# Kernel optimization log

Hardware: AMD Instinct MI355X
Metric: run time of the kernel (lower is better)

## Reference

```python
import jax, jax.numpy as jnp
import numpy as np

B, L, D, H, DH, MAX_SEQ = 2, 2048, 512, 8, 64, 2048


def setup_inputs() -> dict:
    key = jax.random.key(0)
    ks = jax.random.split(key, 9)
    w = 0.02
    return {
        "q": jax.random.normal(ks[0], (B, L, D), jnp.float32),
        "k": jax.random.normal(ks[1], (B, L, D), jnp.float32),
        "v": jax.random.normal(ks[2], (B, L, D), jnp.float32),
        "Wq_w": jax.random.normal(ks[3], (D, D), jnp.float32) * w,
        "Wq_b": jnp.zeros((D,), jnp.float32),
        "Wk_w": jax.random.normal(ks[4], (D, D), jnp.float32) * w,
        "Wk_b": jnp.zeros((D,), jnp.float32),
        "Wv_w": jax.random.normal(ks[5], (D, D), jnp.float32) * w,
        "Wv_b": jnp.zeros((D,), jnp.float32),
        "fc_w": jax.random.normal(ks[6], (D, D), jnp.float32) * w,
        "fc_b": jnp.zeros((D,), jnp.float32),
        "E": jax.random.normal(ks[7], (MAX_SEQ, DH), jnp.float32),
        "mask": jnp.triu(jnp.ones((L, L), jnp.int32), k=1)[None, None],  # 1 = masked
    }


def reference(q, k, v, Wq_w, Wq_b, Wk_w, Wk_b, Wv_w, Wv_b, fc_w, fc_b, E, mask):
    b, lq, d = q.shape

    def proj(x, w, bias):
        # torch Linear: x @ W.T + b, then split heads -> [b, h, l, dh]
        y = x @ w.T + bias
        return y.reshape(b, -1, H, DH).transpose(0, 2, 1, 3)

    qh, kh, vh = proj(q, Wq_w, Wq_b), proj(k, Wk_w, Wk_b), proj(v, Wv_w, Wv_b)
    len_q, len_k = qh.shape[2], kh.shape[2]

    # relative embedding slice (starting_point = max(0, max_seq - len_q))
    e = E[max(0, MAX_SEQ - len_q):, :]          # [m, dh], m == len_q here
    m = e.shape[0]

    QE = jnp.einsum('bhld,md->bhlm', qh, e)      # [b,h,lq,m]
    # qe_masking: keep column j of row i iff j >= m-1-i
    keep = (jnp.arange(m)[None, :] >= (m - 1 - jnp.arange(len_q))[:, None])
    QE = QE * keep.astype(QE.dtype)

    # skewing: left-pad last dim, reshape swapping trailing dims, drop first row
    padded = jnp.pad(QE, ((0, 0), (0, 0), (0, 0), (1, 0)))      # [b,h,lq,m+1]
    Srel = padded.reshape(b, H, m + 1, len_q)[:, :, 1:, :]       # [b,h,m,lq]
    if len_k > len_q:
        Srel = jnp.pad(Srel, ((0, 0), (0, 0), (0, len_k - len_q), (0, 0)))
    elif len_k < len_q:
        Srel = Srel[:, :, :, :len_k]

    QKt = jnp.einsum('bhld,bhmd->bhlm', qh, kh)                  # [b,h,lq,lk]
    logits = (QKt + Srel) / jnp.sqrt(jnp.float32(DH))
    logits = logits + mask.astype(logits.dtype) * jnp.float32(-1e9)
    attn = jax.nn.softmax(logits, axis=-1)
    out = jnp.einsum('bhlm,bhmd->bhld', attn, vh)                # [b,h,lq,dh]
    out = out.transpose(0, 2, 1, 3).reshape(b, len_q, d)
    out = out @ fc_w.T + fc_b
    return out, attn
```

## Files before the change

### kernel.cpp

```cpp
#include <hip/hip_runtime.h>
#include <hip/hip_bf16.h>
#include <cstdint>

typedef __bf16 bf16;
typedef __attribute__((ext_vector_type(8))) __bf16 bf16x8;
typedef __attribute__((ext_vector_type(4))) __bf16 bf16x4;
typedef __attribute__((ext_vector_type(4))) float f32x4;

#define MFMA16 __builtin_amdgcn_mfma_f32_16x16x32_bf16
#define MASKV (-1e30f)

static constexpr int Lq  = 2048;
static constexpr int BKt = 64;

__device__ __forceinline__ void async_load16(const void* g, void* l) {
  __builtin_amdgcn_global_load_lds(
      (__attribute__((address_space(1))) void*)g,
      (__attribute__((address_space(3))) void*)l, 16, 0, 0);
}

__global__ void convert_all(const float* __restrict__ q, const float* __restrict__ k,
                            const float* __restrict__ v, const float* __restrict__ wq,
                            const float* __restrict__ wk, const float* __restrict__ wv,
                            const float* __restrict__ fc, const float* __restrict__ E,
                            bf16* q_bf, bf16* k_bf, bf16* v_bf, bf16* wq_bf,
                            bf16* wk_bf, bf16* wv_bf, bf16* fc_bf, bf16* E_bf)
{
  int i = blockIdx.x * blockDim.x + threadIdx.x;
  const float* src; bf16* dst; int rel;
  if      (i < 524288)  { src = q;  dst = q_bf;  rel = i; }
  else if (i < 1048576) { src = k;  dst = k_bf;  rel = i - 524288; }
  else if (i < 1572864) { src = v;  dst = v_bf;  rel = i - 1048576; }
  else if (i < 1638400) { src = wq; dst = wq_bf; rel = i - 1572864; }
  else if (i < 1703936) { src = wk; dst = wk_bf; rel = i - 1638400; }
  else if (i < 1769472) { src = wv; dst = wv_bf; rel = i - 1703936; }
  else if (i < 1835008) { src = fc; dst = fc_bf; rel = i - 1769472; }
  else if (i < 1867776) { src = E;  dst = E_bf;  rel = i - 1835008; }
  else return;
  float4 x = *(const float4*)(src + (size_t)rel * 4);
  bf16x4 o;
  o[0] = (bf16)x.x; o[1] = (bf16)x.y; o[2] = (bf16)x.z; o[3] = (bf16)x.w;
  *(bf16x4*)(dst + (size_t)rel * 4) = o;
}

__global__ void zero_s(float* __restrict__ s_buf) {
  int i = blockIdx.x * blockDim.x + threadIdx.x;
  if (i < 8192) ((float4*)s_buf)[i] = make_float4(0.f, 0.f, 0.f, 0.f);
}

template<int MODE>
__global__ __launch_bounds__(256, 2)
void gemm512(const bf16* __restrict__ A, const bf16* __restrict__ Bm,
             const float* __restrict__ bias, void* __restrict__ Cv)
{
  __shared__ __align__(16) char lA[16384];
  __shared__ __align__(16) char lB[16384];
  const int tid = threadIdx.x, lane = tid & 63, wv = tid >> 6;
  const int wr = wv >> 1, wc = wv & 1;
  const int tm = blockIdx.x, tn = blockIdx.y;

  f32x4 acc[4][4];
#pragma unroll
  for (int m = 0; m < 4; ++m)
#pragma unroll
    for (int n = 0; n < 4; ++n) acc[m][n] = (f32x4){0.f, 0.f, 0.f, 0.f};

  for (int k0 = 0; k0 < 512; k0 += 64) {
    __syncthreads();
#pragma unroll
    for (int it = 0; it < 4; ++it) {
      int slot = it * 256 + wv * 64 + lane;
      int row = slot >> 3, c = slot & 7;
      int gk = k0 + ((c ^ (row & 7)) * 8);
      async_load16(A  + (size_t)(tm * 128 + row) * 512 + gk, lA + (it * 256 + wv * 64) * 16);
      async_load16(Bm + (size_t)(tn * 128 + row) * 512 + gk, lB + (it * 256 + wv * 64) * 16);
    }
    __syncthreads();
#pragma unroll
    for (int kc = 0; kc < 2; ++kc) {
      bf16x8 af[4], bfr[4];
#pragma unroll
      for (int m = 0; m < 4; ++m) {
        int row = wr * 64 + m * 16 + (lane & 15);
        int ch = ((lane >> 4) + kc * 4) ^ (row & 7);
        af[m] = *(const bf16x8*)(lA + row * 128 + ch * 16);
      }
#pragma unroll
      for (int n = 0; n < 4; ++n) {
        int row = wc * 64 + n * 16 + (lane & 15);
        int ch = ((lane >> 4) + kc * 4) ^ (row & 7);
        bfr[n] = *(const bf16x8*)(lB + row * 128 + ch * 16);
      }
#pragma unroll
      for (int m = 0; m < 4; ++m)
#pragma unroll
        for (int n = 0; n < 4; ++n)
          acc[m][n] = MFMA16(af[m], bfr[n], acc[m][n], 0, 0, 0);
    }
  }

#pragma unroll
  for (int m = 0; m < 4; ++m)
#pragma unroll
    for (int n = 0; n < 4; ++n)
#pragma unroll
      for (int r = 0; r < 4; ++r) {
        int gi = tm * 128 + wr * 64 + m * 16 + 4 * (lane >> 4) + r;
        int gj = tn * 128 + wc * 64 + n * 16 + (lane & 15);
        float vv = acc[m][n][r] + ((MODE == 2) ? bias[gi] : bias[gj]);
        if (MODE == 3) {
          ((float*)Cv)[(size_t)gi * 512 + gj] = vv;
        } else if (MODE == 2) {
          int h = gi >> 6, dh = gi & 63, b = gj >> 11, l = gj & 2047;
          ((bf16*)Cv)[((size_t)((b * 8 + h) * 64 + dh)) * 2048 + l] = (bf16)vv;
        } else {
          int b = gi >> 11, l = gi & 2047, h = gj >> 6, dh = gj & 63;
          ((bf16*)Cv)[((size_t)((b * 8 + h) * 2048 + l)) * 64 + dh] = (bf16)vv;
        }
      }
}

__device__ __forceinline__ void stage_k(const bf16* __restrict__ kb, int j0,
                                        char* dst, int tid) {
#pragma unroll
  for (int it = 0; it < 2; ++it) {
    int slot = it * 256 + tid;
    int row = slot >> 3, c = slot & 7;
    async_load16(kb + (size_t)(j0 + row) * 64 + ((c ^ (row & 7)) * 8), dst + slot * 16);
  }
}
__device__ __forceinline__ void stage_v(const bf16* __restrict__ vb, int j0,
                                        char* dst, int tid) {
#pragma unroll
  for (int it = 0; it < 2; ++it) {
    int slot = it * 256 + tid;
    int row = slot >> 3, c = slot & 7;
    async_load16(vb + (size_t)row * Lq + j0 + ((c ^ (row & 7)) * 8), dst + slot * 16);
  }
}

__device__ __forceinline__ void attn_logits_sh(
    int i0, int j0, int wvx, int lane,
    const bf16x8 qf0, const bf16x8 qf1,
    const bf16* __restrict__ Ebf, const char* lk, f32x4 acc_s[4])
{
  const int rbase = i0 + wvx * 16 - j0 - 63;
  f32x4 acc_t[5];
#pragma unroll
  for (int cf = 0; cf < 5; ++cf) {
    int r = rbase + cf * 16 + (lane & 15);
    int re = 2047 - r; re = re < 0 ? 0 : (re > 2047 ? 2047 : re);
    const bf16* ep = Ebf + (size_t)re * 64 + (lane >> 4) * 8;
    f32x4 a = (f32x4){0.f, 0.f, 0.f, 0.f};
    a = MFMA16(qf0, *(const bf16x8*)ep, a, 0, 0, 0);
    a = MFMA16(qf1, *(const bf16x8*)(ep + 32), a, 0, 0, 0);
    acc_t[cf] = a;
  }
#pragma unroll
  for (int cf = 0; cf < 4; ++cf) {
    int key = cf * 16 + (lane & 15);
    int c0 = (lane >> 4) ^ (key & 7);
    int c1 = ((lane >> 4) + 4) ^ (key & 7);
    f32x4 a = (f32x4){0.f, 0.f, 0.f, 0.f};
    a = MFMA16(qf0, *(const bf16x8*)(lk + key * 128 + c0 * 16), a, 0, 0, 0);
    a = MFMA16(qf1, *(const bf16x8*)(lk + key * 128 + c1 * 16), a, 0, 0, 0);
    acc_s[cf] = a;
  }
  const int g = lane >> 4, b = lane & 15;
#pragma unroll
  for (int r = 0; r < 4; ++r) {
    const int qw  = 4 * g + r;
    const int sl  = (lane & 48) | ((63 + qw - b) & 15);
    const bool hi = qw > b;
#pragma unroll
    for (int cf = 0; cf < 4; ++cf) {
      float vhi = __shfl(acc_t[4 - cf][r], sl);
      float vlo = __shfl(acc_t[3 - cf][r], sl);
      float t = hi ? vhi : vlo;
      float vv = (acc_s[cf][r] + t) * 0.125f;
      if (j0 + cf * 16 + b > i0 + wvx * 16 + qw) vv = MASKV;
      acc_s[cf][r] = vv;
    }
  }
}

__global__ __launch_bounds__(256, 5)
void pass1_sums(const bf16* __restrict__ qh, const bf16* __restrict__ kh,
                const bf16* __restrict__ Ebf, float* __restrict__ s_buf)
{
  __shared__ __align__(16) char lds_k[2][64 * 128];
  const int tid = threadIdx.x, lane = tid & 63, wvx = tid >> 6;
  const int n    = blockIdx.x;
  const int xcd  = n & 7;
  const int r0   = n >> 3;
  const int bh   = 2 * xcd + (r0 & 1);
  int rem = r0 >> 1, qt = 31, f = 0;
#pragma unroll 1
  for (int q = 31; q >= 0; --q) {
    int c = (q >> 2) + 1;
    if (rem < c) { qt = q; f = rem; break; }
    rem -= c;
  }
  const int jbeg = f * 4;
  const int jend = (jbeg + 4 < qt + 1) ? jbeg + 4 : qt + 1;
  const int i0 = qt * 64;

  const bf16* qb = qh + (size_t)bh * Lq * 64;
  const bf16* kb = kh + (size_t)bh * Lq * 64;

  const int qrow = i0 + wvx * 16 + (lane & 15);
  const bf16x8 qf0 = *(const bf16x8*)(qb + (size_t)qrow * 64 + (lane >> 4) * 8);
  const bf16x8 qf1 = *(const bf16x8*)(qb + (size_t)qrow * 64 + 32 + (lane >> 4) * 8);

  f32x4 acc_s[4];
  float s_acc[4] = {0.f, 0.f, 0.f, 0.f};

  stage_k(kb, jbeg * BKt, lds_k[0], tid);
  __syncthreads();
  for (int jt = jbeg; jt < jend; ++jt) {
    const int lt = (jt - jbeg) & 1;
    if (jt + 1 < jend) stage_k(kb, (jt + 1) * BKt, lds_k[lt ^ 1], tid);
    attn_logits_sh(i0, jt * BKt, wvx, lane, qf0, qf1, Ebf, lds_k[lt], acc_s);
#pragma unroll
    for (int r = 0; r < 4; ++r) {
#pragma unroll
      for (int cf = 0; cf < 4; ++cf) s_acc[r] += __expf(acc_s[cf][r]);
    }
    __syncthreads();
  }
#pragma unroll
  for (int r = 0; r < 4; ++r) {
    float s = s_acc[r];
    for (int d = 1; d < 16; d <<= 1) s += __shfl_xor(s, d);
    if ((lane & 15) == 0)
      atomicAdd(&s_buf[bh * Lq + i0 + wvx * 16 + 4 * (lane >> 4) + r], s);
  }
}

__global__ __launch_bounds__(256, 4)
void attn_main(const bf16* __restrict__ qh, const bf16* __restrict__ kh,
               const bf16* __restrict__ vt, const bf16* __restrict__ Ebf,
               const float* __restrict__ s_buf, float* __restrict__ attn_out,
               float* __restrict__ O_slots)
{
  __shared__ __align__(16) char lds_k[2][64 * 128];
  __shared__ __align__(16) char lds_v[2][64 * 128];
  __shared__ __align__(16) char lds_p[4][16 * 64 * 2];

  const int tid = threadIdx.x, lane = tid & 63, wvx = tid >> 6;
  const int n    = blockIdx.x;
  const int xcd  = n & 7;
  const int r0   = n >> 3;
  const int bh   = 2 * xcd + (r0 & 1);
  const int u    = r0 >> 1;
  const int f    = u >> 5;
  const int qt   = u & 31;
  const int i0   = qt * 64;
  const int jbeg = f * 4;
  const int jend = (jbeg + 4 < qt + 1) ? jbeg + 4 : qt + 1;

  float* attn_b = attn_out + (size_t)bh * Lq * Lq;

  if (jbeg <= qt) {
    const bf16* qb = qh + (size_t)bh * Lq * 64;
    const bf16* kb = kh + (size_t)bh * Lq * 64;
    const bf16* vb = vt + (size_t)bh * 64 * Lq;
    bf16* pst = (bf16*)lds_p[wvx];

    const int qrow = i0 + wvx * 16 + (lane & 15);
    const bf16x8 qf0 = *(const bf16x8*)(qb + (size_t)qrow * 64 + (lane >> 4) * 8);
    const bf16x8 qf1 = *(const bf16x8*)(qb + (size_t)qrow * 64 + 32 + (lane >> 4) * 8);

    float inv_s[4];
#pragma unroll
    for (int r = 0; r < 4; ++r)
      inv_s[r] = 1.f / s_buf[bh * Lq + i0 + wvx * 16 + 4 * (lane >> 4) + r];

    f32x4 acc_s[4];
    f32x4 acc_o[4];
#pragma unroll
    for (int nn = 0; nn < 4; ++nn) acc_o[nn] = (f32x4){0.f, 0.f, 0.f, 0.f};

    stage_k(kb, jbeg * BKt, lds_k[0], tid);
    stage_v(vb, jbeg * BKt, lds_v[0], tid);
    __syncthreads();
    for (int jt = jbeg; jt < jend; ++jt) {
      const int j0 = jt * BKt;
      const int lt = (jt - jbeg) & 1;
      if (jt + 1 < jend) {
        stage_k(kb, j0 + BKt, lds_k[lt ^ 1], tid);
        stage_v(vb, j0 + BKt, lds_v[lt ^ 1], tid);
      }
      attn_logits_sh(i0, j0, wvx, lane, qf0, qf1, Ebf, lds_k[lt], acc_s);
#pragma unroll
      for (int cf = 0; cf < 4; ++cf) {
        int kl = cf * 16 + (lane & 15);
        int chs = kl >> 3;
#pragma unroll
        for (int r = 0; r < 4; ++r) {
          int qw = 4 * (lane >> 4) + r;
          float p = __expf(acc_s[cf][r]) * inv_s[r];
          pst[qw * 64 + ((chs ^ (qw & 7)) * 8) + (kl & 7)] = (bf16)p;
        }
      }
      asm volatile("s_waitcnt lgkmcnt(0)" ::: "memory");
      __builtin_amdgcn_sched_barrier(0);
#pragma unroll
      for (int it = 0; it < 2; ++it) {
        int qw = it * 8 + (lane >> 3);
        int c = lane & 7;
        bf16x8 pv = *(const bf16x8*)(pst + qw * 64 + ((c ^ (qw & 7)) * 8));
        float* dst = attn_b + (size_t)(i0 + wvx * 16 + qw) * Lq + j0 + c * 8;
        float4 f0, f1;
        f0.x = (float)pv[0]; f0.y = (float)pv[1]; f0.z = (float)pv[2]; f0.w = (float)pv[3];
        f1.x = (float)pv[4]; f1.y = (float)pv[5]; f1.z = (float)pv[6]; f1.w = (float)pv[7];
        *(float4*)dst = f0; *(float4*)(dst + 4) = f1;
      }
#pragma unroll
      for (int kc = 0; kc < 2; ++kc) {
        int qa = lane & 15;
        int cha = (kc * 4 + (lane >> 4)) ^ (qa & 7);
        bf16x8 pf = *(const bf16x8*)(pst + qa * 64 + cha * 8);
#pragma unroll
        for (int nn = 0; nn < 4; ++nn) {
          int dh = nn * 16 + (lane & 15);
          int chv = (kc * 4 + (lane >> 4)) ^ (dh & 7);
          bf16x8 vf = *(const bf16x8*)(lds_v[lt] + dh * 128 + chv * 16);
          acc_o[nn] = MFMA16(pf, vf, acc_o[nn], 0, 0, 0);
        }
      }
      __syncthreads();
    }

    float* oslot = O_slots + (size_t)(((bh * 32 + qt) * 8 + f)) * 4096;
#pragma unroll
    for (int nn = 0; nn < 4; ++nn)
#pragma unroll
      for (int r = 0; r < 4; ++r) {
        int row = wvx * 16 + 4 * (lane >> 4) + r;
        oslot[row * 64 + nn * 16 + (lane & 15)] = acc_o[nn][r];
      }
  }

  for (int jt = (jbeg > qt + 1 ? jbeg : qt + 1); jt < jbeg + 4; ++jt) {
    const int j0 = jt * BKt;
#pragma unroll
    for (int kk = 0; kk < 4; ++kk) {
      int idx = kk * 256 + tid;
      int row = idx >> 4, c4 = idx & 15;
      float* p = attn_b + (size_t)(i0 + row) * Lq + j0 + c4 * 4;
      *(float4*)p = make_float4(0.f, 0.f, 0.f, 0.f);
    }
  }
}

__global__ void combine_o(const float* __restrict__ O_slots, bf16* __restrict__ oh)
{
  const int sid = blockIdx.x;
  const int bh = sid >> 5, qt = sid & 31;
  const int nch = (qt >> 2) + 1;
  const float* base = O_slots + (size_t)(bh * 32 + qt) * 8 * 4096;
  const int b = bh >> 3, h = bh & 7;
  for (int e4 = threadIdx.x; e4 < 1024; e4 += 256) {
    float4 s = make_float4(0.f, 0.f, 0.f, 0.f);
    for (int ff = 0; ff < nch; ++ff) {
      float4 x = *(const float4*)(base + ff * 4096 + e4 * 4);
      s.x += x.x; s.y += x.y; s.z += x.z; s.w += x.w;
    }
    int row = (e4 * 4) >> 6;
    int col = (e4 * 4) & 63;
    int ig = qt * 64 + row;
    bf16x4 o;
    o[0] = (bf16)s.x; o[1] = (bf16)s.y; o[2] = (bf16)s.z; o[3] = (bf16)s.w;
    *(bf16x4*)(oh + (size_t)(b * 2048 + ig) * 512 + h * 64 + col) = o;
  }
}

extern "C" void kernel_launch(void* const* d_in, const int* in_sizes, int n_in,
                              void* d_out, int out_size, void* d_ws, size_t ws_size,
                              hipStream_t stream) {
  const float* q    = (const float*)d_in[0];
  const float* k    = (const float*)d_in[1];
  const float* v    = (const float*)d_in[2];
  const float* wq   = (const float*)d_in[3];
  const float* wq_b = (const float*)d_in[4];
  const float* wk   = (const float*)d_in[5];
  const float* wk_b = (const float*)d_in[6];
  const float* wv   = (const float*)d_in[7];
  const float* wv_b = (const float*)d_in[8];
  const float* fc   = (const float*)d_in[9];
  const float* fc_b = (const float*)d_in[10];
  const float* E    = (const float*)d_in[11];

  if (ws_size < 98959360) return;
  char* ws = (char*)d_ws;
  bf16*  q_bf    = (bf16*)(ws);
  bf16*  k_bf    = (bf16*)(ws + 4194304);
  bf16*  v_bf    = (bf16*)(ws + 8388608);
  bf16*  wq_bf   = (bf16*)(ws + 12582912);
  bf16*  wk_bf   = (bf16*)(ws + 13107200);
  bf16*  wv_bf   = (bf16*)(ws + 13631488);
  bf16*  fc_bf   = (bf16*)(ws + 14155776);
  bf16*  E_bf    = (bf16*)(ws + 14680064);
  float* s_buf   = (float*)(ws + 14942208);
  bf16*  qh_bf   = (bf16*)(ws + 15073280);
  bf16*  kh_bf   = (bf16*)(ws + 19267584);
  bf16*  vt_bf   = (bf16*)(ws + 23461888);
  bf16*  oh_bf   = (bf16*)(ws + 27656192);
  float* O_slots = (float*)(ws + 31850496);

  float* out_f  = (float*)d_out;
  float* attn_f = out_f + 2097152;

  convert_all<<<7296, 256, 0, stream>>>(q, k, v, wq, wk, wv, fc, E,
      q_bf, k_bf, v_bf, wq_bf, wk_bf, wv_bf, fc_bf, E_bf);
  zero_s<<<32, 256, 0, stream>>>(s_buf);
  gemm512<0><<<dim3(32, 4), 256, 0, stream>>>(q_bf, wq_bf, wq_b, qh_bf);
  gemm512<0><<<dim3(32, 4), 256, 0, stream>>>(k_bf, wk_bf, wk_b, kh_bf);
  gemm512<2><<<dim3(4, 32), 256, 0, stream>>>(wv_bf, v_bf, wv_b, vt_bf);
  pass1_sums<<<2304, 256, 0, stream>>>(qh_bf, kh_bf, E_bf, s_buf);
  attn_main<<<4096, 256, 0, stream>>>(qh_bf, kh_bf, vt_bf, E_bf,
                                      s_buf, attn_f, O_slots);
  combine_o<<<512, 256, 0, stream>>>(O_slots, oh_bf);
  gemm512<3><<<dim3(32, 4), 256, 0, stream>>>(oh_bf, fc_bf, fc_b, out_f);
}
```

Measured before the change: 221.3 us.

## Replace two-pass softmax with unnormalized single pass plus finish normalization kernel

```diff
diff --git a/kernel.cpp b/kernel.cpp
--- a/kernel.cpp
+++ b/kernel.cpp
@@ -24,7 +24,8 @@
                             const float* __restrict__ wk, const float* __restrict__ wv,
                             const float* __restrict__ fc, const float* __restrict__ E,
                             bf16* q_bf, bf16* k_bf, bf16* v_bf, bf16* wq_bf,
-                            bf16* wk_bf, bf16* wv_bf, bf16* fc_bf, bf16* E_bf)
+                            bf16* wk_bf, bf16* wv_bf, bf16* fc_bf, bf16* E_bf,
+                            float* s_buf)
 {
   int i = blockIdx.x * blockDim.x + threadIdx.x;
   const float* src; bf16* dst; int rel;
@@ -36,6 +37,10 @@
   else if (i < 1769472) { src = wv; dst = wv_bf; rel = i - 1703936; }
   else if (i < 1835008) { src = fc; dst = fc_bf; rel = i - 1769472; }
   else if (i < 1867776) { src = E;  dst = E_bf;  rel = i - 1835008; }
+  else if (i < 1875968) {
+    ((float4*)s_buf)[i - 1867776] = make_float4(0.f, 0.f, 0.f, 0.f);
+    return;
+  }
   else return;
   float4 x = *(const float4*)(src + (size_t)rel * 4);
   bf16x4 o;
@@ -43,21 +48,14 @@
   *(bf16x4*)(dst + (size_t)rel * 4) = o;
 }
 
-__global__ void zero_s(float* __restrict__ s_buf) {
-  int i = blockIdx.x * blockDim.x + threadIdx.x;
-  if (i < 8192) ((float4*)s_buf)[i] = make_float4(0.f, 0.f, 0.f, 0.f);
-}
-
 template<int MODE>
-__global__ __launch_bounds__(256, 2)
-void gemm512(const bf16* __restrict__ A, const bf16* __restrict__ Bm,
-             const float* __restrict__ bias, void* __restrict__ Cv)
-{
-  __shared__ __align__(16) char lA[16384];
-  __shared__ __align__(16) char lB[16384];
+__device__ __forceinline__
+void gemm512_core(const bf16* __restrict__ A, const bf16* __restrict__ Bm,
+                  const float* __restrict__ bias, void* __restrict__ Cv,
+                  int tm, int tn, char* lA, char* lB)
+{
   const int tid = threadIdx.x, lane = tid & 63, wv = tid >> 6;
   const int wr = wv >> 1, wc = wv & 1;
-  const int tm = blockIdx.x, tn = blockIdx.y;
 
   f32x4 acc[4][4];
 #pragma unroll
@@ -120,6 +118,31 @@
       }
 }
 
+__global__ __launch_bounds__(256, 2)
+void gemm_qkv(const bf16* __restrict__ q_bf, const bf16* __restrict__ k_bf,
+              const bf16* __restrict__ v_bf, const bf16* __restrict__ wq_bf,
+              const bf16* __restrict__ wk_bf, const bf16* __restrict__ wv_bf,
+              const float* __restrict__ wq_b, const float* __restrict__ wk_b,
+              const float* __restrict__ wv_b,
+              bf16* __restrict__ qh, bf16* __restrict__ kh, bf16* __restrict__ vt)
+{
+  __shared__ __align__(16) char lA[16384];
+  __shared__ __align__(16) char lB[16384];
+  const int z = blockIdx.z;
+  if (z == 0)      gemm512_core<0>(q_bf, wq_bf, wq_b, qh, blockIdx.x, blockIdx.y, lA, lB);
+  else if (z == 1) gemm512_core<0>(k_bf, wk_bf, wk_b, kh, blockIdx.x, blockIdx.y, lA, lB);
+  else             gemm512_core<2>(wv_bf, v_bf, wv_b, vt, blockIdx.y, blockIdx.x, lA, lB);
+}
+
+__global__ __launch_bounds__(256, 2)
+void gemm_fc(const bf16* __restrict__ A, const bf16* __restrict__ Bm,
+             const float* __restrict__ bias, float* __restrict__ Cv)
+{
+  __shared__ __align__(16) char lA[16384];
+  __shared__ __align__(16) char lB[16384];
+  gemm512_core<3>(A, Bm, bias, Cv, blockIdx.x, blockIdx.y, lA, lB);
+}
+
 __device__ __forceinline__ void stage_k(const bf16* __restrict__ kb, int j0,
                                         char* dst, int tid) {
 #pragma unroll
@@ -184,64 +207,11 @@
   }
 }
 
-__global__ __launch_bounds__(256, 5)
-void pass1_sums(const bf16* __restrict__ qh, const bf16* __restrict__ kh,
-                const bf16* __restrict__ Ebf, float* __restrict__ s_buf)
-{
-  __shared__ __align__(16) char lds_k[2][64 * 128];
-  const int tid = threadIdx.x, lane = tid & 63, wvx = tid >> 6;
-  const int n    = blockIdx.x;
-  const int xcd  = n & 7;
-  const int r0   = n >> 3;
-  const int bh   = 2 * xcd + (r0 & 1);
-  int rem = r0 >> 1, qt = 31, f = 0;
-#pragma unroll 1
-  for (int q = 31; q >= 0; --q) {
-    int c = (q >> 2) + 1;
-    if (rem < c) { qt = q; f = rem; break; }
-    rem -= c;
-  }
-  const int jbeg = f * 4;
-  const int jend = (jbeg + 4 < qt + 1) ? jbeg + 4 : qt + 1;
-  const int i0 = qt * 64;
-
-  const bf16* qb = qh + (size_t)bh * Lq * 64;
-  const bf16* kb = kh + (size_t)bh * Lq * 64;
-
-  const int qrow = i0 + wvx * 16 + (lane & 15);
-  const bf16x8 qf0 = *(const bf16x8*)(qb + (size_t)qrow * 64 + (lane >> 4) * 8);
-  const bf16x8 qf1 = *(const bf16x8*)(qb + (size_t)qrow * 64 + 32 + (lane >> 4) * 8);
-
-  f32x4 acc_s[4];
-  float s_acc[4] = {0.f, 0.f, 0.f, 0.f};
-
-  stage_k(kb, jbeg * BKt, lds_k[0], tid);
-  __syncthreads();
-  for (int jt = jbeg; jt < jend; ++jt) {
-    const int lt = (jt - jbeg) & 1;
-    if (jt + 1 < jend) stage_k(kb, (jt + 1) * BKt, lds_k[lt ^ 1], tid);
-    attn_logits_sh(i0, jt * BKt, wvx, lane, qf0, qf1, Ebf, lds_k[lt], acc_s);
-#pragma unroll
-    for (int r = 0; r < 4; ++r) {
-#pragma unroll
-      for (int cf = 0; cf < 4; ++cf) s_acc[r] += __expf(acc_s[cf][r]);
-    }
-    __syncthreads();
-  }
-#pragma unroll
-  for (int r = 0; r < 4; ++r) {
-    float s = s_acc[r];
-    for (int d = 1; d < 16; d <<= 1) s += __shfl_xor(s, d);
-    if ((lane & 15) == 0)
-      atomicAdd(&s_buf[bh * Lq + i0 + wvx * 16 + 4 * (lane >> 4) + r], s);
-  }
-}
-
 __global__ __launch_bounds__(256, 4)
-void attn_main(const bf16* __restrict__ qh, const bf16* __restrict__ kh,
-               const bf16* __restrict__ vt, const bf16* __restrict__ Ebf,
-               const float* __restrict__ s_buf, float* __restrict__ attn_out,
-               float* __restrict__ O_slots)
+void produce(const bf16* __restrict__ qh, const bf16* __restrict__ kh,
+             const bf16* __restrict__ vt, const bf16* __restrict__ Ebf,
+             bf16* __restrict__ P_scr, float* __restrict__ O_slots,
+             float* __restrict__ s_buf)
 {
   __shared__ __align__(16) char lds_k[2][64 * 128];
   __shared__ __align__(16) char lds_v[2][64 * 128];
@@ -258,103 +228,129 @@
   const int i0   = qt * 64;
   const int jbeg = f * 4;
   const int jend = (jbeg + 4 < qt + 1) ? jbeg + 4 : qt + 1;
-
-  float* attn_b = attn_out + (size_t)bh * Lq * Lq;
-
-  if (jbeg <= qt) {
-    const bf16* qb = qh + (size_t)bh * Lq * 64;
-    const bf16* kb = kh + (size_t)bh * Lq * 64;
-    const bf16* vb = vt + (size_t)bh * 64 * Lq;
-    bf16* pst = (bf16*)lds_p[wvx];
-
-    const int qrow = i0 + wvx * 16 + (lane & 15);
-    const bf16x8 qf0 = *(const bf16x8*)(qb + (size_t)qrow * 64 + (lane >> 4) * 8);
-    const bf16x8 qf1 = *(const bf16x8*)(qb + (size_t)qrow * 64 + 32 + (lane >> 4) * 8);
-
-    float inv_s[4];
-#pragma unroll
-    for (int r = 0; r < 4; ++r)
-      inv_s[r] = 1.f / s_buf[bh * Lq + i0 + wvx * 16 + 4 * (lane >> 4) + r];
-
-    f32x4 acc_s[4];
-    f32x4 acc_o[4];
-#pragma unroll
-    for (int nn = 0; nn < 4; ++nn) acc_o[nn] = (f32x4){0.f, 0.f, 0.f, 0.f};
-
-    stage_k(kb, jbeg * BKt, lds_k[0], tid);
-    stage_v(vb, jbeg * BKt, lds_v[0], tid);
+  if (jbeg > qt) return;
+
+  const bf16* qb = qh + (size_t)bh * Lq * 64;
+  const bf16* kb = kh + (size_t)bh * Lq * 64;
+  const bf16* vb = vt + (size_t)bh * 64 * Lq;
+  bf16* P_b = P_scr + (size_t)bh * Lq * Lq;
+  bf16* pst = (bf16*)lds_p[wvx];
+
+  const int qrow = i0 + wvx * 16 + (lane & 15);
+  const bf16x8 qf0 = *(const bf16x8*)(qb + (size_t)qrow * 64 + (lane >> 4) * 8);
+  const bf16x8 qf1 = *(const bf16x8*)(qb + (size_t)qrow * 64 + 32 + (lane >> 4) * 8);
+
+  f32x4 acc_s[4];
+  f32x4 acc_o[4];
+  float s_acc[4] = {0.f, 0.f, 0.f, 0.f};
+#pragma unroll
+  for (int nn = 0; nn < 4; ++nn) acc_o[nn] = (f32x4){0.f, 0.f, 0.f, 0.f};
+
+  stage_k(kb, jbeg * BKt, lds_k[0], tid);
+  stage_v(vb, jbeg * BKt, lds_v[0], tid);
+  __syncthreads();
+  for (int jt = jbeg; jt < jend; ++jt) {
+    const int j0 = jt * BKt;
+    const int lt = (jt - jbeg) & 1;
+    if (jt + 1 < jend) {
+      stage_k(kb, j0 + BKt, lds_k[lt ^ 1], tid);
+      stage_v(vb, j0 + BKt, lds_v[lt ^ 1], tid);
+    }
+    attn_logits_sh(i0, j0, wvx, lane, qf0, qf1, Ebf, lds_k[lt], acc_s);
+#pragma unroll
+    for (int cf = 0; cf < 4; ++cf) {
+      int kl = cf * 16 + (lane & 15);
+      int chs = kl >> 3;
+#pragma unroll
+      for (int r = 0; r < 4; ++r) {
+        int qw = 4 * (lane >> 4) + r;
+        float p = __expf(acc_s[cf][r]);
+        s_acc[r] += p;
+        pst[qw * 64 + ((chs ^ (qw & 7)) * 8) + (kl & 7)] = (bf16)p;
+      }
+    }
+    asm volatile("s_waitcnt lgkmcnt(0)" ::: "memory");
+    __builtin_amdgcn_sched_barrier(0);
+#pragma unroll
+    for (int it = 0; it < 2; ++it) {
+      int qw = it * 8 + (lane >> 3);
+      int c = lane & 7;
+      bf16x8 pv = *(const bf16x8*)(pst + qw * 64 + ((c ^ (qw & 7)) * 8));
+      *(bf16x8*)(P_b + (size_t)(i0 + wvx * 16 + qw) * Lq + j0 + c * 8) = pv;
+    }
+#pragma unroll
+    for (int kc = 0; kc < 2; ++kc) {
+      int qa = lane & 15;
+      int cha = (kc * 4 + (lane >> 4)) ^ (qa & 7);
+      bf16x8 pf = *(const bf16x8*)(pst + qa * 64 + cha * 8);
+#pragma unroll
+      for (int nn = 0; nn < 4; ++nn) {
+        int dh = nn * 16 + (lane & 15);
+        int chv = (kc * 4 + (lane >> 4)) ^ (dh & 7);
+        bf16x8 vf = *(const bf16x8*)(lds_v[lt] + dh * 128 + chv * 16);
+        acc_o[nn] = MFMA16(pf, vf, acc_o[nn], 0, 0, 0);
+      }
+    }
     __syncthreads();
-    for (int jt = jbeg; jt < jend; ++jt) {
-      const int j0 = jt * BKt;
-      const int lt = (jt - jbeg) & 1;
-      if (jt + 1 < jend) {
-        stage_k(kb, j0 + BKt, lds_k[lt ^ 1], tid);
-        stage_v(vb, j0 + BKt, lds_v[lt ^ 1], tid);
-      }
-      attn_logits_sh(i0, j0, wvx, lane, qf0, qf1, Ebf, lds_k[lt], acc_s);
-#pragma unroll
-      for (int cf = 0; cf < 4; ++cf) {
-        int kl = cf * 16 + (lane & 15);
-        int chs = kl >> 3;
-#pragma unroll
-        for (int r = 0; r < 4; ++r) {
-          int qw = 4 * (lane >> 4) + r;
-          float p = __expf(acc_s[cf][r]) * inv_s[r];
-          pst[qw * 64 + ((chs ^ (qw & 7)) * 8) + (kl & 7)] = (bf16)p;
-        }
-      }
-      asm volatile("s_waitcnt lgkmcnt(0)" ::: "memory");
-      __builtin_amdgcn_sched_barrier(0);
-#pragma unroll
-      for (int it = 0; it < 2; ++it) {
-        int qw = it * 8 + (lane >> 3);
-        int c = lane & 7;
-        bf16x8 pv = *(const bf16x8*)(pst + qw * 64 + ((c ^ (qw & 7)) * 8));
-        float* dst = attn_b + (size_t)(i0 + wvx * 16 + qw) * Lq + j0 + c * 8;
-        float4 f0, f1;
-        f0.x = (float)pv[0]; f0.y = (float)pv[1]; f0.z = (float)pv[2]; f0.w = (float)pv[3];
-        f1.x = (float)pv[4]; f1.y = (float)pv[5]; f1.z = (float)pv[6]; f1.w = (float)pv[7];
-        *(float4*)dst = f0; *(float4*)(dst + 4) = f1;
-      }
-#pragma unroll
-      for (int kc = 0; kc < 2; ++kc) {
-        int qa = lane & 15;
-        int cha = (kc * 4 + (lane >> 4)) ^ (qa & 7);
-        bf16x8 pf = *(const bf16x8*)(pst + qa * 64 + cha * 8);
-#pragma unroll
-        for (int nn = 0; nn < 4; ++nn) {
-          int dh = nn * 16 + (lane & 15);
-          int chv = (kc * 4 + (lane >> 4)) ^ (dh & 7);
-          bf16x8 vf = *(const bf16x8*)(lds_v[lt] + dh * 128 + chv * 16);
-          acc_o[nn] = MFMA16(pf, vf, acc_o[nn], 0, 0, 0);
-        }
-      }
-      __syncthreads();
-    }
-
-    float* oslot = O_slots + (size_t)(((bh * 32 + qt) * 8 + f)) * 4096;
-#pragma unroll
-    for (int nn = 0; nn < 4; ++nn)
-#pragma unroll
-      for (int r = 0; r < 4; ++r) {
-        int row = wvx * 16 + 4 * (lane >> 4) + r;
-        oslot[row * 64 + nn * 16 + (lane & 15)] = acc_o[nn][r];
-      }
-  }
-
-  for (int jt = (jbeg > qt + 1 ? jbeg : qt + 1); jt < jbeg + 4; ++jt) {
-    const int j0 = jt * BKt;
-#pragma unroll
-    for (int kk = 0; kk < 4; ++kk) {
-      int idx = kk * 256 + tid;
-      int row = idx >> 4, c4 = idx & 15;
-      float* p = attn_b + (size_t)(i0 + row) * Lq + j0 + c4 * 4;
-      *(float4*)p = make_float4(0.f, 0.f, 0.f, 0.f);
-    }
-  }
-}
-
-__global__ void combine_o(const float* __restrict__ O_slots, bf16* __restrict__ oh)
+  }
+
+  float* oslot = O_slots + (size_t)(((bh * 32 + qt) * 8 + f)) * 4096;
+#pragma unroll
+  for (int nn = 0; nn < 4; ++nn)
+#pragma unroll
+    for (int r = 0; r < 4; ++r) {
+      int row = wvx * 16 + 4 * (lane >> 4) + r;
+      oslot[row * 64 + nn * 16 + (lane & 15)] = acc_o[nn][r];
+    }
+
+#pragma unroll
+  for (int r = 0; r < 4; ++r) {
+    float s = s_acc[r];
+    for (int d = 1; d < 16; d <<= 1) s += __shfl_xor(s, d);
+    if ((lane & 15) == 0)
+      atomicAdd(&s_buf[bh * Lq + i0 + wvx * 16 + 4 * (lane >> 4) + r], s);
+  }
+}
+
+__global__ __launch_bounds__(256, 8)
+void finish(const bf16* __restrict__ P_scr, const float* __restrict__ s_buf,
+            float* __restrict__ attn_out)
+{
+  const int lane = threadIdx.x & 63, wvx = threadIdx.x >> 6;
+  const int row = blockIdx.x * 4 + wvx;
+  const int i   = row & 2047;
+  const float inv = 1.f / s_buf[row];
+  const bf16* src = P_scr + (size_t)row * Lq;
+  float* dst = attn_out + (size_t)row * Lq;
+  const int c0 = lane * 32;
+#pragma unroll
+  for (int k = 0; k < 4; ++k) {
+    const int cb = c0 + k * 8;
+    float4 f0, f1;
+    if (cb + 7 <= i) {
+      bf16x8 pv = *(const bf16x8*)(src + cb);
+      f0.x = (float)pv[0] * inv; f0.y = (float)pv[1] * inv;
+      f0.z = (float)pv[2] * inv; f0.w = (float)pv[3] * inv;
+      f1.x = (float)pv[4] * inv; f1.y = (float)pv[5] * inv;
+      f1.z = (float)pv[6] * inv; f1.w = (float)pv[7] * inv;
+    } else if (cb > i) {
+      f0 = make_float4(0.f, 0.f, 0.f, 0.f);
+      f1 = make_float4(0.f, 0.f, 0.f, 0.f);
+    } else {
+      bf16x8 pv = *(const bf16x8*)(src + cb);
+      float t[8];
+#pragma unroll
+      for (int j = 0; j < 8; ++j) t[j] = (cb + j <= i) ? (float)pv[j] * inv : 0.f;
+      f0.x = t[0]; f0.y = t[1]; f0.z = t[2]; f0.w = t[3];
+      f1.x = t[4]; f1.y = t[5]; f1.z = t[6]; f1.w = t[7];
+    }
+    *(float4*)(dst + cb) = f0;
+    *(float4*)(dst + cb + 4) = f1;
+  }
+}
+
+__global__ void combine_o(const float* __restrict__ O_slots,
+                          const float* __restrict__ s_buf, bf16* __restrict__ oh)
 {
   const int sid = blockIdx.x;
   const int bh = sid >> 5, qt = sid & 31;
@@ -367,11 +363,13 @@
       float4 x = *(const float4*)(base + ff * 4096 + e4 * 4);
       s.x += x.x; s.y += x.y; s.z += x.z; s.w += x.w;
     }
-    int row = (e4 * 4) >> 6;
-    int col = (e4 * 4) & 63;
+    int row = e4 >> 4;
+    int col = (e4 & 15) * 4;
     int ig = qt * 64 + row;
+    float inv = 1.f / s_buf[bh * Lq + ig];
     bf16x4 o;
-    o[0] = (bf16)s.x; o[1] = (bf16)s.y; o[2] = (bf16)s.z; o[3] = (bf16)s.w;
+    o[0] = (bf16)(s.x * inv); o[1] = (bf16)(s.y * inv);
+    o[2] = (bf16)(s.z * inv); o[3] = (bf16)(s.w * inv);
     *(bf16x4*)(oh + (size_t)(b * 2048 + ig) * 512 + h * 64 + col) = o;
   }
 }
@@ -392,7 +390,7 @@
   const float* fc_b = (const float*)d_in[10];
   const float* E    = (const float*)d_in[11];
 
-  if (ws_size < 98959360) return;
+  if (ws_size < 233177088) return;
   char* ws = (char*)d_ws;
   bf16*  q_bf    = (bf16*)(ws);
   bf16*  k_bf    = (bf16*)(ws + 4194304);
@@ -408,19 +406,18 @@
   bf16*  vt_bf   = (bf16*)(ws + 23461888);
   bf16*  oh_bf   = (bf16*)(ws + 27656192);
   float* O_slots = (float*)(ws + 31850496);
+  bf16*  P_scr   = (bf16*)(ws + 98959360);
 
   float* out_f  = (float*)d_out;
   float* attn_f = out_f + 2097152;
 
-  convert_all<<<7296, 256, 0, stream>>>(q, k, v, wq, wk, wv, fc, E,
-      q_bf, k_bf, v_bf, wq_bf, wk_bf, wv_bf, fc_bf, E_bf);
-  zero_s<<<32, 256, 0, stream>>>(s_buf);
-  gemm512<0><<<dim3(32, 4), 256, 0, stream>>>(q_bf, wq_bf, wq_b, qh_bf);
-  gemm512<0><<<dim3(32, 4), 256, 0, stream>>>(k_bf, wk_bf, wk_b, kh_bf);
-  gemm512<2><<<dim3(4, 32), 256, 0, stream>>>(wv_bf, v_bf, wv_b, vt_bf);
-  pass1_sums<<<2304, 256, 0, stream>>>(qh_bf, kh_bf, E_bf, s_buf);
-  attn_main<<<4096, 256, 0, stream>>>(qh_bf, kh_bf, vt_bf, E_bf,
-                                      s_buf, attn_f, O_slots);
-  combine_o<<<512, 256, 0, stream>>>(O_slots, oh_bf);
-  gemm512<3><<<dim3(32, 4), 256, 0, stream>>>(oh_bf, fc_bf, fc_b, out_f);
-}
+  convert_all<<<7328, 256, 0, stream>>>(q, k, v, wq, wk, wv, fc, E,
+      q_bf, k_bf, v_bf, wq_bf, wk_bf, wv_bf, fc_bf, E_bf, s_buf);
+  gemm_qkv<<<dim3(32, 4, 3), 256, 0, stream>>>(q_bf, k_bf, v_bf,
+      wq_bf, wk_bf, wv_bf, wq_b, wk_b, wv_b, qh_bf, kh_bf, vt_bf);
+  produce<<<4096, 256, 0, stream>>>(qh_bf, kh_bf, vt_bf, E_bf,
+                                    P_scr, O_slots, s_buf);
+  finish<<<8192, 256, 0, stream>>>(P_scr, s_buf, attn_f);
+  combine_o<<<512, 256, 0, stream>>>(O_slots, s_buf, oh_bf);
+  gemm_fc<<<dim3(32, 4), 256, 0, stream>>>(oh_bf, fc_bf, fc_b, out_f);
+}
```

Result: slower. 337.8 us (+52.7%).
